# Kernel optimization log

Hardware: AMD Instinct MI355X
Metric: run time of the kernel (lower is better)

The kernel has to match this reference:

```python
import jax, jax.numpy as jnp
import numpy as np

B, C, N, K = 16, 128, 1024, 16
QK_DIM, V_DIM = 64, 128


def setup_inputs() -> dict:
    key = jax.random.key(0)
    k1, k2, k3, k4, k5 = jax.random.split(key, 5)
    return {
        "input_tensor": jax.random.normal(k1, (B, C, N, K), dtype=jnp.float32),
        "W_qk": jax.random.normal(k2, (2 * QK_DIM, C), dtype=jnp.float32) * 0.05,
        "b_qk": jax.random.normal(k3, (2 * QK_DIM,), dtype=jnp.float32) * 0.01,
        "W_v": jax.random.normal(k4, (V_DIM, C), dtype=jnp.float32) * 0.05,
        "b_v": jax.random.normal(k5, (V_DIM,), dtype=jnp.float32) * 0.01,
        "qk_dim": QK_DIM,
    }


def reference(input_tensor, W_qk, b_qk, W_v, b_v, qk_dim):
    # 1x1 conv == channel matmul: [B,C,N,K] x [2*qk,C] -> [B,2*qk,N,K]
    combine = jnp.einsum('bcnk,oc->bonk', input_tensor, W_qk) + b_qk[None, :, None, None]
    q = combine[:, :qk_dim]          # [B, qk, N, K]
    k = combine[:, qk_dim:]          # [B, qk, N, K]
    # per-point attention over neighbor axis
    energy = jnp.einsum('bcnq,bcnk->bnqk', q, k)            # [B, N, K, K]
    scale = jnp.asarray(qk_dim, energy.dtype) ** 0.5
    attention = jax.nn.softmax(energy / scale, axis=3)       # softmax over last k
    v = jnp.einsum('bcnk,oc->bonk', input_tensor, W_v) + b_v[None, :, None, None]  # [B, v, N, K]
    attention_first = attention[:, :, :, 0]                  # [B, N, K] (q-axis slice at k=0)
    # out = einsum('bnk,bcnk->bnkc') then sum over k -> fuse into one einsum
    output = jnp.einsum('bnk,bcnk->bnc', attention_first, v) # [B, N, v_dim]
    return output
```

## Files before the change

kernel.cpp:

```cpp
#include <hip/hip_runtime.h>
#include <stdint.h>

typedef __attribute__((ext_vector_type(4))) float f32x4;
typedef __attribute__((ext_vector_type(8))) short s16x8;

__device__ __forceinline__ unsigned int f2bf_u(float x) {
  union { float f; unsigned int u; } v; v.f = x;
  return (v.u + 0x7FFFu + ((v.u >> 16) & 1u)) >> 16;
}
__device__ __forceinline__ unsigned int pack_bf2(float lo, float hi) {
  return f2bf_u(lo) | (f2bf_u(hi) << 16);
}
__device__ __forceinline__ float bflo(unsigned int w) { return __uint_as_float(w << 16); }
__device__ __forceinline__ float bfhi(unsigned int w) { return __uint_as_float(w & 0xFFFF0000u); }

union FragU { uint4 u; s16x8 s; };

__global__ void __launch_bounds__(256) prep_weights(const float* __restrict__ Wqk,
                                                    const float* __restrict__ Wv,
                                                    uint16_t* __restrict__ wsqk,
                                                    uint16_t* __restrict__ wsv) {
  int i = blockIdx.x * 256 + threadIdx.x;
  if (i < 16384) {
    wsqk[i] = (uint16_t)f2bf_u(Wqk[i]);
  } else if (i < 32768) {
    int j = i - 16384;
    wsv[j] = (uint16_t)f2bf_u(Wv[j]);
  }
}

__global__ void __launch_bounds__(256, 6) attn_kernel(
    const float* __restrict__ X,
    const float* __restrict__ bqk,
    const float* __restrict__ bv,
    const unsigned int* __restrict__ wqk,
    const unsigned int* __restrict__ wv,
    float* __restrict__ out)
{
  __shared__ unsigned int sXt[64 * 66];
  __shared__ unsigned int sY[4 * 68];
  __shared__ float sa[4][16];
  __shared__ float sS[4];

  const int t    = threadIdx.x;
  const int lane = t & 63;
  const int w    = t >> 6;
  const int nn   = lane & 15;
  const int quad = lane >> 4;

  const int blk = blockIdx.x;
  const int b   = blk >> 8;
  const int n0  = (blk & 255) << 2;

  {
    const int j4 = nn;
    const int q  = quad;
    const float* Xg = X + (size_t)b * (128 * 1024 * 16) + (size_t)n0 * 16;
    #pragma unroll
    for (int it = 0; it < 8; ++it) {
      const int cbase = it * 16 + w * 4;
      const int c = cbase + q;
      float4 V = *reinterpret_cast<const float4*>(Xg + (size_t)c * 16384 + j4 * 4);
      {
        const bool Q0 = (q >> 1) == 0;
        float a  = Q0 ? V.z : V.x;
        float bb = Q0 ? V.w : V.y;
        a  = __shfl_xor(a, 32);
        bb = __shfl_xor(bb, 32);
        if (Q0) { V.z = a; V.w = bb; } else { V.x = a; V.y = bb; }
      }
      {
        const bool q0 = (q & 1) == 0;
        float a  = q0 ? V.y : V.x;
        float bb = q0 ? V.w : V.z;
        a  = __shfl_xor(a, 16);
        bb = __shfl_xor(bb, 16);
        if (q0) { V.y = a; V.w = bb; } else { V.x = a; V.z = bb; }
      }
      const int j = 4 * j4 + q;
      uint2 pk;
      pk.x = pack_bf2(V.x, V.y);
      pk.y = pack_bf2(V.z, V.w);
      *reinterpret_cast<uint2*>(&sXt[j * 66 + (cbase >> 1)]) = pk;
    }
  }
  __syncthreads();

  const int jrow = w * 16 + nn;

  f32x4 e; e[0] = 0.f; e[1] = 0.f; e[2] = 0.f; e[3] = 0.f;
  const int src0 = nn + ((quad & 1) << 5);
  const int src1 = src0 + 16;
  const bool hi  = (quad >> 1) != 0;

  #pragma unroll
  for (int h = 0; h < 2; ++h) {
    f32x4 acc[4];
    #pragma unroll
    for (int i = 0; i < 4; ++i) {
      const int ot = (i < 2) ? (2 * h + i) : (4 + 2 * h + (i - 2));
      const float4 bq = *reinterpret_cast<const float4*>(bqk + ot * 16 + quad * 4);
      acc[i][0] = bq.x; acc[i][1] = bq.y; acc[i][2] = bq.z; acc[i][3] = bq.w;
    }
    #pragma unroll
    for (int ks = 0; ks < 4; ++ks) {
      FragU bfrag;
      bfrag.u = *reinterpret_cast<const uint4*>(&sXt[jrow * 66 + ks * 16 + quad * 4]);
      #pragma unroll
      for (int i = 0; i < 4; ++i) {
        const int ot = (i < 2) ? (2 * h + i) : (4 + 2 * h + (i - 2));
        FragU af;
        af.u = *reinterpret_cast<const uint4*>(wqk + (ot * 16 + nn) * 64 + ks * 16 + quad * 4);
        acc[i] = __builtin_amdgcn_mfma_f32_16x16x32_bf16(af.s, bfrag.s, acc[i], 0, 0, 0);
      }
    }
    unsigned int w01[4], w23[4];
    #pragma unroll
    for (int i = 0; i < 4; ++i) {
      w01[i] = pack_bf2(acc[i][0], acc[i][1]);
      w23[i] = pack_bf2(acc[i][2], acc[i][3]);
    }
    FragU qf, kf;
    {
      unsigned int a0 = __shfl(w01[0], src0, 64), b0 = __shfl(w01[1], src0, 64);
      unsigned int a1 = __shfl(w23[0], src0, 64), b1 = __shfl(w23[1], src0, 64);
      unsigned int a2 = __shfl(w01[0], src1, 64), b2 = __shfl(w01[1], src1, 64);
      unsigned int a3 = __shfl(w23[0], src1, 64), b3 = __shfl(w23[1], src1, 64);
      qf.u.x = hi ? b0 : a0; qf.u.y = hi ? b1 : a1;
      qf.u.z = hi ? b2 : a2; qf.u.w = hi ? b3 : a3;
    }
    {
      unsigned int a0 = __shfl(w01[2], src0, 64), b0 = __shfl(w01[3], src0, 64);
      unsigned int a1 = __shfl(w23[2], src0, 64), b1 = __shfl(w23[3], src0, 64);
      unsigned int a2 = __shfl(w01[2], src1, 64), b2 = __shfl(w01[3], src1, 64);
      unsigned int a3 = __shfl(w23[2], src1, 64), b3 = __shfl(w23[3], src1, 64);
      kf.u.x = hi ? b0 : a0; kf.u.y = hi ? b1 : a1;
      kf.u.z = hi ? b2 : a2; kf.u.w = hi ? b3 : a3;
    }
    e = __builtin_amdgcn_mfma_f32_16x16x32_bf16(qf.s, kf.s, e, 0, 0, 0);
  }

  {
    float p[4], sm[4];
    #pragma unroll
    for (int rr = 0; rr < 4; ++rr) {
      float l = e[rr] * 0.125f;
      float mx = l;
      mx = fmaxf(mx, __shfl_xor(mx, 1));
      mx = fmaxf(mx, __shfl_xor(mx, 2));
      mx = fmaxf(mx, __shfl_xor(mx, 4));
      mx = fmaxf(mx, __shfl_xor(mx, 8));
      float pe = __expf(l - mx);
      float ss = pe;
      ss += __shfl_xor(ss, 1);
      ss += __shfl_xor(ss, 2);
      ss += __shfl_xor(ss, 4);
      ss += __shfl_xor(ss, 8);
      p[rr] = pe; sm[rr] = ss;
    }
    if (nn == 0) {
      #pragma unroll
      for (int rr = 0; rr < 4; ++rr) sa[w][quad * 4 + rr] = p[rr] / sm[rr];
    }
  }

  {
    float a[16];
    float S = 0.f;
    #pragma unroll
    for (int k = 0; k < 16; ++k) { a[k] = sa[w][k]; S += a[k]; }
    float y0 = 0.f, y1 = 0.f;
    #pragma unroll
    for (int k = 0; k < 16; ++k) {
      const unsigned int xw = sXt[(w * 16 + k) * 66 + lane];
      y0 += a[k] * bflo(xw);
      y1 += a[k] * bfhi(xw);
    }
    sY[w * 68 + lane] = pack_bf2(y0, y1);
    if (lane == 0) sS[w] = S;
  }
  __syncthreads();

  {
    #pragma unroll
    for (int i = 0; i < 2; ++i) {
      const int ct = w * 2 + i;
      f32x4 z; z[0] = 0.f; z[1] = 0.f; z[2] = 0.f; z[3] = 0.f;
      #pragma unroll
      for (int ks = 0; ks < 4; ++ks) {
        FragU av, by;
        av.u = *reinterpret_cast<const uint4*>(wv + (ct * 16 + nn) * 64 + ks * 16 + quad * 4);
        uint4 tmp; tmp.x = 0u; tmp.y = 0u; tmp.z = 0u; tmp.w = 0u;
        if (nn < 4) tmp = *reinterpret_cast<const uint4*>(&sY[nn * 68 + ks * 16 + quad * 4]);
        by.u = tmp;
        z = __builtin_amdgcn_mfma_f32_16x16x32_bf16(av.s, by.s, z, 0, 0, 0);
      }
      if (nn < 4) {
        const float4 bvv = *reinterpret_cast<const float4*>(bv + ct * 16 + quad * 4);
        const float S = sS[nn];
        float4 o4;
        o4.x = z[0] + bvv.x * S;
        o4.y = z[1] + bvv.y * S;
        o4.z = z[2] + bvv.z * S;
        o4.w = z[3] + bvv.w * S;
        *reinterpret_cast<float4*>(out + (size_t)(b * 1024 + n0 + nn) * 128 + ct * 16 + quad * 4) = o4;
      }
    }
  }
}

extern "C" void kernel_launch(void* const* d_in, const int* in_sizes, int n_in,
                              void* d_out, int out_size, void* d_ws, size_t ws_size,
                              hipStream_t stream) {
  (void)in_sizes; (void)n_in; (void)out_size; (void)ws_size;
  const float* X   = (const float*)d_in[0];
  const float* Wqk = (const float*)d_in[1];
  const float* bqk = (const float*)d_in[2];
  const float* Wv  = (const float*)d_in[3];
  const float* bv  = (const float*)d_in[4];

  uint16_t* wsqk = (uint16_t*)d_ws;
  uint16_t* wsv  = wsqk + 16384;

  prep_weights<<<128, 256, 0, stream>>>(Wqk, Wv, wsqk, wsv);
  attn_kernel<<<4096, 256, 0, stream>>>(X, bqk, bv,
                                        (const unsigned int*)wsqk,
                                        (const unsigned int*)wsv,
                                        (float*)d_out);
}
```

Measured before the change: 259.2 us.

## Split QK projection by output rows across waves and exchange via LDS

Each wave now computes a 16-row output slice of the Q/K projection for all 64 neighbor columns, reusing one weight fragment across four MFMAs instead of loading four weight fragments per k-step. Results are packed to bf16 and written to a new shared transpose buffer, then reread per point to build the Q and K fragments for the energy MFMA, replacing the cross-lane shuffles. This cuts global/L2 weight traffic per wave at the cost of extra LDS usage, LDS writes, and two added block barriers per tile.

```diff
diff --git a/kernel.cpp b/kernel.cpp
--- a/kernel.cpp
+++ b/kernel.cpp
@@ -38,6 +38,7 @@
     float* __restrict__ out)
 {
   __shared__ unsigned int sXt[64 * 66];
+  __shared__ unsigned int sPt[64 * 34];
   __shared__ unsigned int sY[4 * 68];
   __shared__ float sa[4][16];
   __shared__ float sS[4];
@@ -86,58 +87,56 @@
   }
   __syncthreads();
 
-  const int jrow = w * 16 + nn;
-
   f32x4 e; e[0] = 0.f; e[1] = 0.f; e[2] = 0.f; e[3] = 0.f;
-  const int src0 = nn + ((quad & 1) << 5);
-  const int src1 = src0 + 16;
-  const bool hi  = (quad >> 1) != 0;
 
   #pragma unroll
   for (int h = 0; h < 2; ++h) {
+    const int O       = (w < 2) ? (32 * h + 16 * w) : (64 + 32 * h + 16 * (w - 2));
+    const int colbase = (w < 2) ? (8 * w)           : (16 + 8 * (w - 2));
     f32x4 acc[4];
-    #pragma unroll
-    for (int i = 0; i < 4; ++i) {
-      const int ot = (i < 2) ? (2 * h + i) : (4 + 2 * h + (i - 2));
-      const float4 bq = *reinterpret_cast<const float4*>(bqk + ot * 16 + quad * 4);
-      acc[i][0] = bq.x; acc[i][1] = bq.y; acc[i][2] = bq.z; acc[i][3] = bq.w;
+    {
+      const float4 bq = *reinterpret_cast<const float4*>(bqk + O + quad * 4);
+      #pragma unroll
+      for (int tt = 0; tt < 4; ++tt) {
+        acc[tt][0] = bq.x; acc[tt][1] = bq.y; acc[tt][2] = bq.z; acc[tt][3] = bq.w;
+      }
     }
     #pragma unroll
     for (int ks = 0; ks < 4; ++ks) {
-      FragU bfrag;
-      bfrag.u = *reinterpret_cast<const uint4*>(&sXt[jrow * 66 + ks * 16 + quad * 4]);
-      #pragma unroll
-      for (int i = 0; i < 4; ++i) {
-        const int ot = (i < 2) ? (2 * h + i) : (4 + 2 * h + (i - 2));
-        FragU af;
-        af.u = *reinterpret_cast<const uint4*>(wqk + (ot * 16 + nn) * 64 + ks * 16 + quad * 4);
-        acc[i] = __builtin_amdgcn_mfma_f32_16x16x32_bf16(af.s, bfrag.s, acc[i], 0, 0, 0);
-      }
-    }
-    unsigned int w01[4], w23[4];
-    #pragma unroll
-    for (int i = 0; i < 4; ++i) {
-      w01[i] = pack_bf2(acc[i][0], acc[i][1]);
-      w23[i] = pack_bf2(acc[i][2], acc[i][3]);
-    }
-    FragU qf, kf;
+      FragU af, bf[4];
+      af.u = *reinterpret_cast<const uint4*>(wqk + (O + nn) * 64 + ks * 16 + quad * 4);
+      #pragma unroll
+      for (int tt = 0; tt < 4; ++tt)
+        bf[tt].u = *reinterpret_cast<const uint4*>(&sXt[(tt * 16 + nn) * 66 + ks * 16 + quad * 4]);
+      #pragma unroll
+      for (int tt = 0; tt < 4; ++tt)
+        acc[tt] = __builtin_amdgcn_mfma_f32_16x16x32_bf16(af.s, bf[tt].s, acc[tt], 0, 0, 0);
+    }
+    #pragma unroll
+    for (int tt = 0; tt < 4; ++tt) {
+      const int j = tt * 16 + nn;
+      const unsigned int pw0 = pack_bf2(acc[tt][0], acc[tt][1]);
+      const unsigned int pw1 = pack_bf2(acc[tt][2], acc[tt][3]);
+      #pragma unroll
+      for (int s = 0; s < 2; ++s) {
+        const int rp = (nn + s) & 1;
+        sPt[j * 34 + colbase + quad * 2 + rp] = rp ? pw1 : pw0;
+      }
+    }
+    __syncthreads();
+
     {
-      unsigned int a0 = __shfl(w01[0], src0, 64), b0 = __shfl(w01[1], src0, 64);
-      unsigned int a1 = __shfl(w23[0], src0, 64), b1 = __shfl(w23[1], src0, 64);
-      unsigned int a2 = __shfl(w01[0], src1, 64), b2 = __shfl(w01[1], src1, 64);
-      unsigned int a3 = __shfl(w23[0], src1, 64), b3 = __shfl(w23[1], src1, 64);
-      qf.u.x = hi ? b0 : a0; qf.u.y = hi ? b1 : a1;
-      qf.u.z = hi ? b2 : a2; qf.u.w = hi ? b3 : a3;
-    }
-    {
-      unsigned int a0 = __shfl(w01[2], src0, 64), b0 = __shfl(w01[3], src0, 64);
-      unsigned int a1 = __shfl(w23[2], src0, 64), b1 = __shfl(w23[3], src0, 64);
-      unsigned int a2 = __shfl(w01[2], src1, 64), b2 = __shfl(w01[3], src1, 64);
-      unsigned int a3 = __shfl(w23[2], src1, 64), b3 = __shfl(w23[3], src1, 64);
-      kf.u.x = hi ? b0 : a0; kf.u.y = hi ? b1 : a1;
-      kf.u.z = hi ? b2 : a2; kf.u.w = hi ? b3 : a3;
-    }
-    e = __builtin_amdgcn_mfma_f32_16x16x32_bf16(qf.s, kf.s, e, 0, 0, 0);
+      const int row = (w * 16 + nn) * 34;
+      FragU qf, kf;
+      const uint2 qlo = *reinterpret_cast<const uint2*>(&sPt[row + quad * 4]);
+      const uint2 qhi = *reinterpret_cast<const uint2*>(&sPt[row + quad * 4 + 2]);
+      const uint2 klo = *reinterpret_cast<const uint2*>(&sPt[row + 16 + quad * 4]);
+      const uint2 khi = *reinterpret_cast<const uint2*>(&sPt[row + 16 + quad * 4 + 2]);
+      qf.u.x = qlo.x; qf.u.y = qlo.y; qf.u.z = qhi.x; qf.u.w = qhi.y;
+      kf.u.x = klo.x; kf.u.y = klo.y; kf.u.z = khi.x; kf.u.w = khi.y;
+      e = __builtin_amdgcn_mfma_f32_16x16x32_bf16(qf.s, kf.s, e, 0, 0, 0);
+    }
+    if (h == 0) __syncthreads();
   }
 
   {
```

Result: faster. 218.8 us (-15.6%).
